# Kernel tuning notes

Hardware: AMD Instinct MI355X
Metric: run time of the kernel (lower is better)

The kernel has to match this reference:

```python
import jax, jax.numpy as jnp
import numpy as np

N, T, F = 4096, 24, 16          # nodes, seq_len, in_features
H = 128                          # temporal_hidden
NH, DO = 4, 32                   # gat num_heads, gat out_features (NH*DO == H)
SEM, PH = 64, 32                 # semantic hidden, predictor hidden
SLOPE = 0.2                      # leaky_relu negative slope
ADJ_P = 0.01                     # adjacency density


def setup_inputs() -> dict:
    key = jax.random.key(0)
    ks = jax.random.split(key, 40)
    f32 = jnp.float32

    def rn(k, shape, s=0.02):
        return jax.random.normal(k, shape, f32) * s

    features = jax.random.normal(ks[0], (N, T, F), f32)
    pos_adj = (jax.random.uniform(ks[1], (N, N)) < ADJ_P).astype(f32)
    neg_adj = (jax.random.uniform(ks[2], (N, N)) < ADJ_P).astype(f32)

    inp = dict(features=features, pos_adj=pos_adj, neg_adj=neg_adj)
    # GRU (torch layout: W_ih [3H,F], W_hh [3H,H], gate order r,z,n)
    inp['gru_Wih'] = rn(ks[3], (3 * H, F), 1.0 / np.sqrt(H))
    inp['gru_Whh'] = rn(ks[4], (3 * H, H), 1.0 / np.sqrt(H))
    inp['gru_bih'] = rn(ks[5], (3 * H,), 1.0 / np.sqrt(H))
    inp['gru_bhh'] = rn(ks[6], (3 * H,), 1.0 / np.sqrt(H))
    # GAT params (linear weights stored [in, out] so we use x @ W)
    i = 7
    for pre in ('pos', 'neg'):
        inp[pre + '_W'] = rn(ks[i], (H, NH * DO)); i += 1
        inp[pre + '_u'] = rn(ks[i], (NH, DO, 1), 1.0); i += 1
        inp[pre + '_v'] = rn(ks[i], (NH, DO, 1), 1.0); i += 1
        inp[pre + '_b'] = rn(ks[i], (1, NH * DO)); i += 1
        inp[pre + '_pW'] = rn(ks[i], (H, NH * DO)); i += 1
        inp[pre + '_pb'] = jnp.zeros((NH * DO,), f32)
    inp['self_W'] = rn(ks[i], (H, H)); i += 1
    inp['self_b'] = jnp.zeros((H,), f32)
    inp['mpos_W'] = rn(ks[i], (NH * DO, H)); i += 1
    inp['mpos_b'] = jnp.zeros((H,), f32)
    inp['mneg_W'] = rn(ks[i], (NH * DO, H)); i += 1
    inp['mneg_b'] = jnp.zeros((H,), f32)
    inp['sem_W1'] = rn(ks[i], (H, SEM)); i += 1
    inp['sem_b1'] = jnp.zeros((SEM,), f32)
    inp['sem_W2'] = rn(ks[i], (SEM, 1)); i += 1
    inp['pred_W1'] = rn(ks[i], (H, PH)); i += 1
    inp['pred_b1'] = jnp.zeros((PH,), f32)
    inp['pred_W2'] = rn(ks[i], (PH, 1)); i += 1
    inp['pred_b2'] = jnp.zeros((1,), f32)
    return inp


def _gru_last(x, Wih, Whh, bih, bhh):
    # x: [N, T, F] -> last hidden state [N, H]
    gi_all = jnp.einsum('ntf,gf->tng', x, Wih) + bih  # precompute input gates [T,N,3H]
    h0 = jnp.zeros((x.shape[0], Whh.shape[1]), x.dtype)

    def step(h, gi):
        gh = h @ Whh.T + bhh
        ir, iz, in_ = jnp.split(gi, 3, axis=-1)
        hr, hz, hn = jnp.split(gh, 3, axis=-1)
        r = jax.nn.sigmoid(ir + hr)
        z = jax.nn.sigmoid(iz + hz)
        n = jnp.tanh(in_ + r * hn)
        return (1.0 - z) * n + z * h, None

    h, _ = jax.lax.scan(step, h0, gi_all)
    return h


def _gat(x, adj, W, u, v, b, pW, pb):
    sup = (x @ W).reshape(-1, NH, DO).transpose(1, 0, 2)     # [NH, N, DO]
    f1 = jnp.matmul(sup, u).reshape(NH, 1, -1)               # [NH, 1, N]
    f2 = jnp.matmul(sup, v).reshape(NH, -1, 1)               # [NH, N, 1]
    w = jax.nn.leaky_relu(f1 + f2, SLOPE)                    # [NH, N, N]
    mw = w * adj                                             # mask
    rs = mw.sum(axis=2, keepdims=True)
    rs = jnp.where(rs == 0, jnp.ones_like(rs), rs)
    attn = mw / rs
    out = jnp.matmul(attn, sup).transpose(1, 0, 2).reshape(-1, NH * DO)
    return out + b + x @ pW + pb                             # bias + residual


def _pairnorm_si(x):
    x = x - x.mean(axis=0)
    rn = jnp.sqrt(1e-6 + (x * x).sum(axis=1, keepdims=True))
    return x / rn


def reference(features, pos_adj, neg_adj,
              gru_Wih, gru_Whh, gru_bih, gru_bhh,
              pos_W, pos_u, pos_v, pos_b, pos_pW, pos_pb,
              neg_W, neg_u, neg_v, neg_b, neg_pW, neg_pb,
              self_W, self_b, mpos_W, mpos_b, mneg_W, mneg_b,
              sem_W1, sem_b1, sem_W2,
              pred_W1, pred_b1, pred_W2, pred_b2):
    support = _gru_last(features, gru_Wih, gru_Whh, gru_bih, gru_bhh)  # [N, H]
    pos_sup = _gat(support, pos_adj, pos_W, pos_u, pos_v, pos_b, pos_pW, pos_pb)
    neg_sup = _gat(support, neg_adj, neg_W, neg_u, neg_v, neg_b, neg_pW, neg_pb)
    self_e = support @ self_W + self_b
    pos_e = pos_sup @ mpos_W + mpos_b
    neg_e = neg_sup @ mneg_W + mneg_b
    emb = jnp.stack([self_e, pos_e, neg_e], axis=1)          # [N, 3, H]
    w = jnp.tanh(emb @ sem_W1 + sem_b1) @ sem_W2             # [N, 3, 1]
    beta = jax.nn.softmax(w, axis=1)
    fused = (beta * emb).sum(axis=1)                          # [N, H]
    fused = _pairnorm_si(fused)
    h = jax.nn.relu(fused @ pred_W1 + pred_b1)               # dropout is eval no-op
    out = jax.nn.sigmoid(h @ pred_W2 + pred_b2).squeeze(-1)  # [N]
    return out
```

## Files before the change

### kernel.cpp

```cpp
#include <hip/hip_runtime.h>


#define NN 4096

typedef unsigned short u16;
typedef unsigned int   u32;
typedef unsigned long long u64;
typedef __attribute__((ext_vector_type(8))) short  short8;
typedef __attribute__((ext_vector_type(4))) float  float4v;

__device__ inline float bf2f(u16 u){ return __uint_as_float(((u32)u)<<16); }
__device__ inline u16 f2bf(float f){
  u32 x = __float_as_uint(f);
  return (u16)((x + 0x7fffu + ((x>>16)&1u))>>16);
}
__device__ inline float ldm(const void* p, int i, int bf){
  return bf ? bf2f(((const u16*)p)[i]) : ((const float*)p)[i];
}
__device__ inline u16 ldm16(const void* p, int i, int bf){
  return bf ? ((const u16*)p)[i] : f2bf(((const float*)p)[i]);
}
__device__ inline float fexp(float x){
  x = fminf(fmaxf(x,-80.f),80.f);
  return __builtin_amdgcn_exp2f(x*1.4426950408889634f);
}
__device__ inline float sigm(float x){
  return __builtin_amdgcn_rcpf(1.f + fexp(-x));
}
__device__ inline float tanhf_(float x){
  float c = fminf(fmaxf(x,-15.f),15.f);
  float e = __builtin_amdgcn_exp2f(c*2.8853900817779268f);
  return (e-1.f)*__builtin_amdgcn_rcpf(e+1.f);
}
__device__ inline float4v mfma16(short8 a, short8 b, float4v c){
  return __builtin_amdgcn_mfma_f32_16x16x32_bf16(a,b,c,0,0,0);
}
__device__ inline int rdbf(const int* __restrict__ mflag){
  int b=0;
  #pragma unroll
  for (int k=0;k<16;k++) b|=mflag[k];
  return b;
}

__global__ __launch_bounds__(256) void k_detect(const u32* __restrict__ adj,
                                                int* __restrict__ mflag)
{
  __shared__ u32 w4[4];
  const int lane=threadIdx.x&63, wv=threadIdx.x>>6;
  int i = (blockIdx.x*256 + threadIdx.x)*4;
  uint4 v = *(const uint4*)(adj + i);
  u32 acc = (v.x | v.y | v.z | v.w) & 0xFFFFu;
  unsigned long long b = __ballot(acc != 0);
  if (lane==0) w4[wv] = (b!=0);
  __syncthreads();
  if (threadIdx.x==0) mflag[blockIdx.x] = (w4[0]|w4[1]|w4[2]|w4[3]) ? 1 : 0;
}

__global__ __launch_bounds__(256) void k_imp(
  const int* __restrict__ mflag,
  const void* gWih, const void* gWhh, const void* gbih, const void* gbhh,
  const void* posW, const void* posu, const void* posv, const void* posb,
  const void* pospW, const void* pospb,
  const void* negW, const void* negu, const void* negv, const void* negb,
  const void* negpW, const void* negpb,
  const void* selfW, const void* selfb, const void* mposW, const void* mposb,
  const void* mnegW, const void* mnegb,
  const void* semW1, const void* semb1, const void* semW2,
  const void* predW1, const void* predb1, const void* predW2, const void* predb2,
  u16* __restrict__ Wihb, u16* __restrict__ Whhb,
  u16* __restrict__ WT1,  u16* __restrict__ WT2,
  float* __restrict__ cbrz, float* __restrict__ cbin, float* __restrict__ cbhn,
  float* __restrict__ cuv,  float* __restrict__ cgb,  float* __restrict__ csb,
  float* __restrict__ cw1,  float* __restrict__ cb1,  float* __restrict__ cw2,
  float* __restrict__ cpw1, float* __restrict__ cpb1, float* __restrict__ cpw2,
  float* __restrict__ cpb2, float* __restrict__ meanacc)
{
  const int bf = rdbf(mflag);
  int i = blockIdx.x*256 + threadIdx.x;
  if (i < 6144){ Wihb[i]=ldm16(gWih,i,bf); return; }  i-=6144;
  if (i < 49152){ Whhb[i]=ldm16(gWhh,i,bf); return; } i-=49152;
  if (i < 81920){
    int m=i>>7,k=i&127,sel=m>>7,ml=m&127;
    const void* s = sel==0?posW: sel==1?pospW: sel==2?negW: sel==3?negpW: selfW;
    WT1[i]=ldm16(s,k*128+ml,bf); return;
  } i-=81920;
  if (i < 32768){
    int m=i>>7,k=i&127;
    const void* s = (m<128)? mposW : mnegW;
    WT2[i]=ldm16(s,k*128+(m&127),bf); return;
  } i-=32768;
  if (i < 256){ cbrz[i]=ldm(gbih,i,bf)+ldm(gbhh,i,bf); return; } i-=256;
  if (i < 128){ cbin[i]=ldm(gbih,256+i,bf); return; } i-=128;
  if (i < 128){ cbhn[i]=ldm(gbhh,256+i,bf); return; } i-=128;
  if (i < 512){
    int s=i>>8, rem=i&255, wh=rem>>7, hd=rem&127;
    const void* p = s? (wh? negv:negu) : (wh? posv:posu);
    cuv[i]=ldm(p,hd,bf); return;
  } i-=512;
  if (i < 256){
    int s=i>>7, d=i&127;
    cgb[i]=ldm(s?negb:posb,d,bf)+ldm(s?negpb:pospb,d,bf); return;
  } i-=256;
  if (i < 384){
    int t=i>>7, d=i&127;
    const void* p = t==0? selfb : t==1? mposb : mnegb;
    csb[i]=ldm(p,d,bf); return;
  } i-=384;
  if (i < 8192){ cw1[i]=ldm(semW1,i,bf); return; } i-=8192;
  if (i < 64){ cb1[i]=ldm(semb1,i,bf); return; } i-=64;
  if (i < 64){ cw2[i]=ldm(semW2,i,bf); return; } i-=64;
  if (i < 4096){ cpw1[i]=ldm(predW1,i,bf); return; } i-=4096;
  if (i < 32){ cpb1[i]=ldm(predb1,i,bf); return; } i-=32;
  if (i < 32){ cpw2[i]=ldm(predW2,i,bf); return; } i-=32;
  if (i < 1){ cpb2[i]=ldm(predb2,i,bf); return; } i-=1;
  if (i < 128){ meanacc[i]=0.f; return; }
}

__global__ __launch_bounds__(512) void k_fat1(
  const int* __restrict__ mflag,
  const void* posadj, const void* negadj,
  int* __restrict__ deg, u16* __restrict__ idx,
  const void* feat,
  const u16* __restrict__ Wihb, const u16* __restrict__ Whhb,
  const float* __restrict__ cbrz, const float* __restrict__ cbin,
  const float* __restrict__ cbhn,
  const u16* __restrict__ WT1, const float* __restrict__ cuv,
  float* __restrict__ C1, float* __restrict__ f12)
{
  __shared__ __attribute__((aligned(16))) u16 sh_x[16*392];
  __shared__ __attribute__((aligned(16))) u16 hbuf[2][16*136];
  const int bf = rdbf(mflag);
  const int tid=threadIdx.x, lane=tid&63, wv=tid>>6;
  const int bx=blockIdx.x;

  if (bx < 1024){
    const int gid = bx*8 + wv;
    const int s = gid>>12, row = gid&4095;
    const void* adj = s? negadj : posadj;
    u64 mask = 0;
    if (bf){
      const u16* rp = (const u16*)adj + (size_t)row*4096;
      #pragma unroll
      for (int it=0; it<8; it++){
        const uint4 vv = *(const uint4*)(rp + it*512 + lane*8);
        u32 w[4]={vv.x,vv.y,vv.z,vv.w};
        #pragma unroll
        for (int q=0;q<4;q++){
          if (w[q]&0xffffu) mask |= 1ull<<(it*8+2*q);
          if (w[q]>>16)     mask |= 1ull<<(it*8+2*q+1);
        }
      }
    } else {
      const float* rp = (const float*)adj + (size_t)row*4096;
      #pragma unroll
      for (int it=0; it<16; it++){
        const uint4 vv = *(const uint4*)(rp + it*256 + lane*4);
        if (vv.x) mask |= 1ull<<(it*4+0);
        if (vv.y) mask |= 1ull<<(it*4+1);
        if (vv.z) mask |= 1ull<<(it*4+2);
        if (vv.w) mask |= 1ull<<(it*4+3);
      }
    }
    int cnt = __popcll(mask);
    int pre = cnt;
    #pragma unroll
    for (int off=1; off<64; off<<=1){
      int o = __shfl_up(pre, off);
      if (lane>=off) pre += o;
    }
    int base_p = pre - cnt;
    int total = __shfl(pre, 63);
    u16* out = idx + ((size_t)s*NN + row)*128;
    u64 mm = mask; int k = 0;
    while (mm){
      int b = __ffsll(mm)-1; mm &= mm-1;
      int e = bf ? ((b>>3)*512 + lane*8 + (b&7))
                 : ((b>>2)*256 + lane*4 + (b&3));
      int p = base_p + k; k++;
      if (p<128) out[p] = (u16)e;
    }
    if (lane==0) deg[s*NN+row] = total>128 ? 128 : total;
    return;
  }

  const int quad=lane>>4, c15=lane&15;
  const int n0=(bx-1024)*16;

  if (bf){
    const u16* f16p=(const u16*)feat;
    for (int i=tid;i<16*384;i+=512){ int n=i/384,e=i-n*384; sh_x[n*392+e]=f16p[(size_t)(n0+n)*384+e]; }
  } else {
    const float* f32p=(const float*)feat;
    for (int i=tid;i<16*384;i+=512){ int n=i/384,e=i-n*384; sh_x[n*392+e]=f2bf(f32p[(size_t)(n0+n)*384+e]); }
  }
  for (int i=tid;i<16*136;i+=512) hbuf[0][i]=0;

  const short8 z8={0,0,0,0,0,0,0,0};
  const float4v z4={0.f,0.f,0.f,0.f};
  short8 bh[3][4], bx3[3];
  #pragma unroll
  for (int g=0;g<3;g++){
    int rowb=(g*8+wv)*16+c15;
    #pragma unroll
    for (int ks=0;ks<4;ks++) bh[g][ks]=*(const short8*)(Whhb+(size_t)rowb*128+ks*32+quad*8);
    bx3[g] = (quad<2)? *(const short8*)(Wihb+(size_t)rowb*16+quad*8) : z8;
  }
  const int j0=wv*16+c15;
  const float brz_r=cbrz[j0], brz_z=cbrz[128+j0];
  const float bin0=cbin[j0],  bhn0=cbhn[j0];
  float hr[4]={0.f,0.f,0.f,0.f};
  __syncthreads();

  for (int t=0;t<24;t++){
    const u16* hb  = hbuf[t&1];
    u16*       hbn = hbuf[(t+1)&1];
    short8 ah[4];
    #pragma unroll
    for (int ks=0;ks<4;ks++) ah[ks]=*(const short8*)(hb + c15*136 + ks*32 + quad*8);
    short8 ax = (quad<2)? *(const short8*)(sh_x + c15*392 + t*16 + quad*8) : z8;
    float4v racc = mfma16(ax,bx3[0],z4);
    float4v zacc = mfma16(ax,bx3[1],z4);
    float4v ni   = mfma16(ax,bx3[2],z4);
    float4v nh   = z4;
    #pragma unroll
    for (int ks=0;ks<4;ks++){
      racc = mfma16(ah[ks],bh[0][ks],racc);
      zacc = mfma16(ah[ks],bh[1][ks],zacc);
      nh   = mfma16(ah[ks],bh[2][ks],nh);
    }
    #pragma unroll
    for (int rr=0;rr<4;rr++){
      const int node = quad*4+rr;
      float r_ = sigm(racc[rr]+brz_r);
      float z_ = sigm(zacc[rr]+brz_z);
      float n_ = tanhf_(ni[rr]+bin0 + r_*(nh[rr]+bhn0));
      float hv = (1.f-z_)*n_ + z_*hr[rr];
      hr[rr]=hv; hbn[node*136+j0]=f2bf(hv);
    }
    __syncthreads();
  }
  short8 a[4];
  #pragma unroll
  for (int ks=0;ks<4;ks++) a[ks]=*(const short8*)(hbuf[0]+c15*136+ks*32+quad*8);
  #pragma unroll
  for (int q=0;q<5;q++){
    int tile=wv*5+q;
    float4v acc={0.f,0.f,0.f,0.f};
    #pragma unroll
    for (int ks=0;ks<4;ks++){
      short8 b=*(const short8*)(WT1+(size_t)(tile*16+c15)*128+ks*32+quad*8);
      acc=mfma16(a[ks],b,acc);
    }
    #pragma unroll
    for (int r=0;r<4;r++) C1[(size_t)(n0+quad*4+r)*640 + tile*16 + c15]=acc[r];
  }
  __syncthreads();
  {
    int q=tid;
    int nl=q&15, h=(q>>4)&3, wsel=(q>>6)&1, s=(q>>7)&1;
    const float* uvp = cuv + s*256 + wsel*128 + h*32;
    const float* SL  = C1 + (size_t)(n0+nl)*640 + s*256 + h*32;
    float t=0.f;
    #pragma unroll
    for (int d=0;d<32;d++) t += SL[d]*uvp[d];
    f12[s*32768 + wsel*16384 + h*4096 + (n0+nl)] = t;
  }
}

__global__ __launch_bounds__(1024) void k_fat2(
  const float* __restrict__ C1, const float* __restrict__ f12,
  const int* __restrict__ deg, const u16* __restrict__ idx,
  const float* __restrict__ cgb, const u16* __restrict__ WT2,
  float* __restrict__ E)
{
  __shared__ u16   nbuf[16][128];
  __shared__ float wbuf[16][4][128];
  __shared__ __attribute__((aligned(16))) u16 sA[16*136];
  const int s=blockIdx.y;
  const int wv=threadIdx.x>>6, lane=threadIdx.x&63;
  const int n0=blockIdx.x*16;
  const int i=n0+wv;
  const int d0=lane, d1=lane+64, h0=lane>>5, h1=2+(lane>>5);
  const float* f1 = f12 + s*32768;
  const float* f2 = f12 + s*32768 + 16384;
  const int dgr = deg[s*NN+i];
  const int dg  = dgr>128 ? 128 : dgr;
  const u16* nb = idx + ((size_t)s*NN+i)*128;
  ((u32*)nbuf[wv])[lane] = ((const u32*)nb)[lane];
  float f2v[4];
  #pragma unroll
  for (int h=0;h<4;h++) f2v[h]=f2[h*4096+i];
  for (int e=lane; e<dg; e+=64){
    int j = nbuf[wv][e];
    #pragma unroll
    for (int h=0;h<4;h++){
      float w = f1[h*4096+j] + f2v[h];
      wbuf[wv][h][e] = w>0.f ? w : 0.2f*w;
    }
  }
  float acc0=0.f,acc1=0.f,rs0=0.f,rs1=0.f;
  #pragma unroll 4
  for (int e=0;e<dg;e++){
    float w0 = wbuf[wv][h0][e];
    float w1 = wbuf[wv][h1][e];
    int j = nbuf[wv][e];
    const float* SL = C1 + (size_t)j*640 + s*256;
    acc0 += w0*SL[d0]; rs0 += w0;
    acc1 += w1*SL[d1]; rs1 += w1;
  }
  if (rs0==0.f) rs0=1.f;
  if (rs1==0.f) rs1=1.f;
  const float* P = C1 + (size_t)i*640 + s*256 + 128;
  sA[wv*136+d0]=f2bf(acc0/rs0 + cgb[s*128+d0] + P[d0]);
  sA[wv*136+d1]=f2bf(acc1/rs1 + cgb[s*128+d1] + P[d1]);
  __syncthreads();
  if (wv<8){
    const int quad=lane>>4, c15=lane&15;
    short8 a[4];
    #pragma unroll
    for (int ks=0;ks<4;ks++) a[ks]=*(const short8*)(sA+c15*136+ks*32+quad*8);
    const int tile=wv;
    float4v acc={0.f,0.f,0.f,0.f};
    #pragma unroll
    for (int ks=0;ks<4;ks++){
      short8 b=*(const short8*)(WT2+(size_t)(s*128+tile*16+c15)*128+ks*32+quad*8);
      acc=mfma16(a[ks],b,acc);
    }
    #pragma unroll
    for (int r=0;r<4;r++) E[(size_t)(n0+quad*4+r)*256 + s*128 + tile*16 + c15]=acc[r];
  }
}

__global__ __launch_bounds__(256) void k_sem(
  const float* __restrict__ C1, const float* __restrict__ E,
  const float* __restrict__ csb, const float* __restrict__ cw1,
  const float* __restrict__ cb1, const float* __restrict__ cw2,
  float* __restrict__ fused, float* __restrict__ meanacc)
{
  __shared__ float sW1[128*64];
  __shared__ float sW2[64];
  __shared__ float sb1[64];
  __shared__ float sE[4][3][128];
  const int tid=threadIdx.x, wv=tid>>6, lane=tid&63;
  for (int i=tid;i<8192;i+=256) sW1[i]=cw1[i];
  if (tid<64){ sW2[tid]=cw2[tid]; sb1[tid]=cb1[tid]; }
  const int n = blockIdx.x*4 + wv;
  for (int d=lane; d<128; d+=64){
    sE[wv][0][d] = C1[(size_t)n*640+512+d] + csb[d];
    sE[wv][1][d] = E[(size_t)n*256 + d]    + csb[128+d];
    sE[wv][2][d] = E[(size_t)n*256+128+d]  + csb[256+d];
  }
  __syncthreads();
  float sc[3];
  #pragma unroll
  for (int s=0;s<3;s++){
    float t = sb1[lane];
    for (int k=0;k<128;k++) t += sE[wv][s][k]*sW1[k*64+lane];
    t = tanhf_(t);
    float p = t*sW2[lane];
    #pragma unroll
    for (int off=32; off; off>>=1) p += __shfl_xor(p, off);
    sc[s]=p;
  }
  float mx = fmaxf(sc[0], fmaxf(sc[1],sc[2]));
  float e0=fexp(sc[0]-mx), e1=fexp(sc[1]-mx), e2=fexp(sc[2]-mx);
  float inv = 1.f/(e0+e1+e2);
  float b0=e0*inv, b1=e1*inv, b2=e2*inv;
  float fv[2];
  for (int h=0; h<2; h++){
    int d=lane+h*64;
    fv[h] = b0*sE[wv][0][d] + b1*sE[wv][1][d] + b2*sE[wv][2][d];
    fused[(size_t)n*128+d] = fv[h];
  }
  __syncthreads();
  for (int h=0; h<2; h++) sE[wv][0][lane+h*64] = fv[h];
  __syncthreads();
  if (tid<128)
    atomicAdd(&meanacc[tid], sE[0][0][tid]+sE[1][0][tid]+sE[2][0][tid]+sE[3][0][tid]);
}

__global__ __launch_bounds__(256) void k_pred(
  const float* __restrict__ fused, const float* __restrict__ meanacc,
  const float* __restrict__ cpw1, const float* __restrict__ cpb1,
  const float* __restrict__ cpw2, const float* __restrict__ cpb2,
  float* __restrict__ out)
{
  __shared__ float sy[4][128];
  __shared__ float sW1[128*32];
  __shared__ float sW2[32];
  const int tid=threadIdx.x, wv=tid>>6, lane=tid&63;
  for (int i=tid;i<4096;i+=256) sW1[i]=cpw1[i];
  if (tid<32) sW2[tid]=cpw2[tid];
  const int n = blockIdx.x*4 + wv;
  const float inv_n = 1.f/4096.f;
  float x0 = fused[(size_t)n*128+lane]    - meanacc[lane]*inv_n;
  float x1 = fused[(size_t)n*128+64+lane] - meanacc[64+lane]*inv_n;
  float ss = x0*x0 + x1*x1;
  #pragma unroll
  for (int o=32;o;o>>=1) ss += __shfl_xor(ss,o);
  float ir = 1.f/sqrtf(1e-6f + ss);
  sy[wv][lane]=x0*ir; sy[wv][64+lane]=x1*ir;
  __syncthreads();
  float h=0.f;
  if (lane<32){
    h = cpb1[lane];
    for (int k=0;k<128;k++) h += sy[wv][k]*sW1[k*32+lane];
    h = h>0.f? h : 0.f;
    h = h*sW2[lane];
  }
  #pragma unroll
  for (int o=32;o;o>>=1) h += __shfl_xor(h,o);
  if (!lane){
    float z = h + cpb2[0];
    out[n] = __builtin_amdgcn_rcpf(1.f + fexp(-z));
  }
}

extern "C" void kernel_launch(void* const* d_in, const int* in_sizes, int n_in,
                              void* d_out, int out_size, void* d_ws, size_t ws_size,
                              hipStream_t stream)
{
  const void* feat  =d_in[0];
  const void* posadj=d_in[1];
  const void* negadj=d_in[2];
  const void* gWih  =d_in[3];
  const void* gWhh  =d_in[4];
  const void* gbih  =d_in[5];
  const void* gbhh  =d_in[6];
  const void* posW  =d_in[7];
  const void* posu  =d_in[8];
  const void* posv  =d_in[9];
  const void* posb  =d_in[10];
  const void* pospW =d_in[11];
  const void* pospb =d_in[12];
  const void* negW  =d_in[13];
  const void* negu  =d_in[14];
  const void* negv  =d_in[15];
  const void* negb  =d_in[16];
  const void* negpW =d_in[17];
  const void* negpb =d_in[18];
  const void* selfW =d_in[19];
  const void* selfb =d_in[20];
  const void* mposW =d_in[21];
  const void* mposb =d_in[22];
  const void* mnegW =d_in[23];
  const void* mnegb =d_in[24];
  const void* semW1 =d_in[25];
  const void* semb1 =d_in[26];
  const void* semW2 =d_in[27];
  const void* predW1=d_in[28];
  const void* predb1=d_in[29];
  const void* predW2=d_in[30];
  const void* predb2=d_in[31];

  char* wsb=(char*)d_ws; size_t off=0;
  auto alloc=[&](size_t bytes)->void*{ void* p=wsb+off; off+=(bytes+255)&~(size_t)255; return p; };
  int*   mflag=(int*)  alloc(256);
  u16*   Wihb =(u16*)  alloc(6144*2);
  u16*   Whhb =(u16*)  alloc(49152*2);
  u16*   WT1  =(u16*)  alloc(81920*2);
  u16*   WT2  =(u16*)  alloc(32768*2);
  float* cbrz =(float*)alloc(256*4);
  float* cbin =(float*)alloc(128*4);
  float* cbhn =(float*)alloc(128*4);
  float* cuv  =(float*)alloc(512*4);
  float* cgb  =(float*)alloc(256*4);
  float* csb  =(float*)alloc(384*4);
  float* cw1  =(float*)alloc(8192*4);
  float* cb1  =(float*)alloc(64*4);
  float* cw2  =(float*)alloc(64*4);
  float* cpw1 =(float*)alloc(4096*4);
  float* cpb1 =(float*)alloc(32*4);
  float* cpw2 =(float*)alloc(32*4);
  float* cpb2 =(float*)alloc(4);
  float* C1   =(float*)alloc((size_t)NN*640*4);
  float* f12  =(float*)alloc((size_t)65536*4);
  int*   deg  =(int*)  alloc((size_t)2*NN*4);
  u16*   nidx =(u16*)  alloc((size_t)2*NN*128*2);
  float* E    =(float*)alloc((size_t)NN*256*4);
  float* fused=(float*)alloc((size_t)NN*128*4);
  float* meanacc=(float*)alloc(128*4);
  (void)ws_size; (void)in_sizes; (void)n_in; (void)out_size;

  k_detect<<<16,          256,0,stream>>>((const u32*)posadj,mflag);
  k_imp   <<<720,         256,0,stream>>>(mflag,gWih,gWhh,gbih,gbhh,
              posW,posu,posv,posb,pospW,pospb,negW,negu,negv,negb,negpW,negpb,
              selfW,selfb,mposW,mposb,mnegW,mnegb,semW1,semb1,semW2,
              predW1,predb1,predW2,predb2,
              Wihb,Whhb,WT1,WT2,cbrz,cbin,cbhn,cuv,cgb,csb,cw1,cb1,cw2,
              cpw1,cpb1,cpw2,cpb2,meanacc);
  k_fat1  <<<1280,        512,0,stream>>>(mflag,posadj,negadj,deg,nidx,
              feat,Wihb,Whhb,cbrz,cbin,cbhn,WT1,cuv,C1,f12);
  k_fat2  <<<dim3(256,2),1024,0,stream>>>(C1,f12,deg,nidx,cgb,WT2,E);
  k_sem   <<<NN/4,        256,0,stream>>>(C1,E,csb,cw1,cb1,cw2,fused,meanacc);
  k_pred  <<<NN/4,        256,0,stream>>>(fused,meanacc,cpw1,cpb1,cpw2,cpb2,(float*)d_out);
}
```

Measured before the change: 318.8 us.

## Split CSR build from GRU kernel, store C1 in bf16, vectorize sem/pred matvecs

Adjacency-to-neighbour-list extraction moves into its own kernel. Each wave scans half a row and reserves output slots with an atomicAdd on deg, which k_detect now zeroes. The GRU/projection kernel writes the C1 intermediate as bf16 instead of fp32, halving its store and gather traffic in the GAT and semantic kernels. The semantic and predictor weights are pre-transposed with padding so the matvecs use float4 LDS reads, and k_sem handles four nodes per wave with a block-level mean reduction. The costs are extra bf16 rounding, nondeterministic neighbour order, no clamp on deg at 128, and losing the overlap between CSR building and GRU work that the fused launch gave.

```diff
diff --git a/kernel.cpp b/kernel.cpp
--- a/kernel.cpp
+++ b/kernel.cpp
@@ -43,7 +43,8 @@
 }
 
 __global__ __launch_bounds__(256) void k_detect(const u32* __restrict__ adj,
-                                                int* __restrict__ mflag)
+                                                int* __restrict__ mflag,
+                                                int* __restrict__ deg)
 {
   __shared__ u32 w4[4];
   const int lane=threadIdx.x&63, wv=threadIdx.x>>6;
@@ -52,6 +53,8 @@
   u32 acc = (v.x | v.y | v.z | v.w) & 0xFFFFu;
   unsigned long long b = __ballot(acc != 0);
   if (lane==0) w4[wv] = (b!=0);
+  deg[blockIdx.x*512 + threadIdx.x] = 0;
+  deg[blockIdx.x*512 + threadIdx.x + 256] = 0;
   __syncthreads();
   if (threadIdx.x==0) mflag[blockIdx.x] = (w4[0]|w4[1]|w4[2]|w4[3]) ? 1 : 0;
 }
@@ -71,8 +74,8 @@
   u16* __restrict__ WT1,  u16* __restrict__ WT2,
   float* __restrict__ cbrz, float* __restrict__ cbin, float* __restrict__ cbhn,
   float* __restrict__ cuv,  float* __restrict__ cgb,  float* __restrict__ csb,
-  float* __restrict__ cw1,  float* __restrict__ cb1,  float* __restrict__ cw2,
-  float* __restrict__ cpw1, float* __restrict__ cpb1, float* __restrict__ cpw2,
+  float* __restrict__ cw1t, float* __restrict__ cb1,  float* __restrict__ cw2,
+  float* __restrict__ cpw1t, float* __restrict__ cpb1, float* __restrict__ cpw2,
   float* __restrict__ cpb2, float* __restrict__ meanacc)
 {
   const int bf = rdbf(mflag);
@@ -106,85 +109,92 @@
     const void* p = t==0? selfb : t==1? mposb : mnegb;
     csb[i]=ldm(p,d,bf); return;
   } i-=384;
-  if (i < 8192){ cw1[i]=ldm(semW1,i,bf); return; } i-=8192;
+  if (i < 8448){
+    int c=i/132, k=i-c*132;
+    cw1t[i] = (k<128)? ldm(semW1,k*64+c,bf) : 0.f; return;
+  } i-=8448;
   if (i < 64){ cb1[i]=ldm(semb1,i,bf); return; } i-=64;
   if (i < 64){ cw2[i]=ldm(semW2,i,bf); return; } i-=64;
-  if (i < 4096){ cpw1[i]=ldm(predW1,i,bf); return; } i-=4096;
+  if (i < 4224){
+    int c=i/132, k=i-c*132;
+    cpw1t[i] = (k<128)? ldm(predW1,k*32+c,bf) : 0.f; return;
+  } i-=4224;
   if (i < 32){ cpb1[i]=ldm(predb1,i,bf); return; } i-=32;
   if (i < 32){ cpw2[i]=ldm(predW2,i,bf); return; } i-=32;
   if (i < 1){ cpb2[i]=ldm(predb2,i,bf); return; } i-=1;
   if (i < 128){ meanacc[i]=0.f; return; }
 }
 
-__global__ __launch_bounds__(512) void k_fat1(
+__global__ __launch_bounds__(256) void k_csr(
   const int* __restrict__ mflag,
   const void* posadj, const void* negadj,
-  int* __restrict__ deg, u16* __restrict__ idx,
-  const void* feat,
+  int* __restrict__ deg, u16* __restrict__ idx)
+{
+  const int bf = rdbf(mflag);
+  const int s = blockIdx.y;
+  const void* adj = s? negadj : posadj;
+  const int lane = threadIdx.x&63;
+  const int hr   = blockIdx.x*4 + (threadIdx.x>>6);
+  const int row  = hr>>1, half = hr&1;
+  u32 mask = 0;
+  if (bf){
+    const u16* rp = (const u16*)adj + (size_t)row*4096 + half*2048;
+    #pragma unroll
+    for (int q=0;q<4;q++){
+      uint4 v = *(const uint4*)(rp + q*512 + lane*8);
+      if (v.x&0xffffu) mask|=1u<<(q*8+0); if (v.x>>16) mask|=1u<<(q*8+1);
+      if (v.y&0xffffu) mask|=1u<<(q*8+2); if (v.y>>16) mask|=1u<<(q*8+3);
+      if (v.z&0xffffu) mask|=1u<<(q*8+4); if (v.z>>16) mask|=1u<<(q*8+5);
+      if (v.w&0xffffu) mask|=1u<<(q*8+6); if (v.w>>16) mask|=1u<<(q*8+7);
+    }
+  } else {
+    const float* rp = (const float*)adj + (size_t)row*4096 + half*2048;
+    #pragma unroll
+    for (int q=0;q<8;q++){
+      uint4 v = *(const uint4*)(rp + q*256 + lane*4);
+      if (v.x) mask|=1u<<(q*4+0);
+      if (v.y) mask|=1u<<(q*4+1);
+      if (v.z) mask|=1u<<(q*4+2);
+      if (v.w) mask|=1u<<(q*4+3);
+    }
+  }
+  int cnt = __popc(mask);
+  int pre = cnt;
+  #pragma unroll
+  for (int off=1; off<64; off<<=1){
+    int o = __shfl_up(pre, off);
+    if (lane>=off) pre += o;
+  }
+  int tot = __shfl(pre, 63);
+  int wbase = 0;
+  if (lane==0) wbase = atomicAdd(&deg[s*NN+row], tot);
+  wbase = __shfl(wbase, 0);
+  int base_p = wbase + pre - cnt;
+  u16* out = idx + ((size_t)s*NN + row)*128;
+  u32 mm = mask; int k = 0;
+  while (mm){
+    int b = __ffs(mm)-1; mm &= mm-1;
+    int e = bf ? (half*2048 + (b>>3)*512 + lane*8 + (b&7))
+               : (half*2048 + (b>>2)*256 + lane*4 + (b&3));
+    int p = base_p + k; k++;
+    if (p<128) out[p] = (u16)e;
+  }
+}
+
+__global__ __launch_bounds__(512) void k_gruf(
+  const int* __restrict__ mflag, const void* feat,
   const u16* __restrict__ Wihb, const u16* __restrict__ Whhb,
   const float* __restrict__ cbrz, const float* __restrict__ cbin,
   const float* __restrict__ cbhn,
   const u16* __restrict__ WT1, const float* __restrict__ cuv,
-  float* __restrict__ C1, float* __restrict__ f12)
+  u16* __restrict__ C1b, float* __restrict__ f12)
 {
   __shared__ __attribute__((aligned(16))) u16 sh_x[16*392];
   __shared__ __attribute__((aligned(16))) u16 hbuf[2][16*136];
   const int bf = rdbf(mflag);
   const int tid=threadIdx.x, lane=tid&63, wv=tid>>6;
-  const int bx=blockIdx.x;
-
-  if (bx < 1024){
-    const int gid = bx*8 + wv;
-    const int s = gid>>12, row = gid&4095;
-    const void* adj = s? negadj : posadj;
-    u64 mask = 0;
-    if (bf){
-      const u16* rp = (const u16*)adj + (size_t)row*4096;
-      #pragma unroll
-      for (int it=0; it<8; it++){
-        const uint4 vv = *(const uint4*)(rp + it*512 + lane*8);
-        u32 w[4]={vv.x,vv.y,vv.z,vv.w};
-        #pragma unroll
-        for (int q=0;q<4;q++){
-          if (w[q]&0xffffu) mask |= 1ull<<(it*8+2*q);
-          if (w[q]>>16)     mask |= 1ull<<(it*8+2*q+1);
-        }
-      }
-    } else {
-      const float* rp = (const float*)adj + (size_t)row*4096;
-      #pragma unroll
-      for (int it=0; it<16; it++){
-        const uint4 vv = *(const uint4*)(rp + it*256 + lane*4);
-        if (vv.x) mask |= 1ull<<(it*4+0);
-        if (vv.y) mask |= 1ull<<(it*4+1);
-        if (vv.z) mask |= 1ull<<(it*4+2);
-        if (vv.w) mask |= 1ull<<(it*4+3);
-      }
-    }
-    int cnt = __popcll(mask);
-    int pre = cnt;
-    #pragma unroll
-    for (int off=1; off<64; off<<=1){
-      int o = __shfl_up(pre, off);
-      if (lane>=off) pre += o;
-    }
-    int base_p = pre - cnt;
-    int total = __shfl(pre, 63);
-    u16* out = idx + ((size_t)s*NN + row)*128;
-    u64 mm = mask; int k = 0;
-    while (mm){
-      int b = __ffsll(mm)-1; mm &= mm-1;
-      int e = bf ? ((b>>3)*512 + lane*8 + (b&7))
-                 : ((b>>2)*256 + lane*4 + (b&3));
-      int p = base_p + k; k++;
-      if (p<128) out[p] = (u16)e;
-    }
-    if (lane==0) deg[s*NN+row] = total>128 ? 128 : total;
-    return;
-  }
-
   const int quad=lane>>4, c15=lane&15;
-  const int n0=(bx-1024)*16;
+  const int n0=blockIdx.x*16;
 
   if (bf){
     const u16* f16p=(const u16*)feat;
@@ -252,23 +262,24 @@
       acc=mfma16(a[ks],b,acc);
     }
     #pragma unroll
-    for (int r=0;r<4;r++) C1[(size_t)(n0+quad*4+r)*640 + tile*16 + c15]=acc[r];
+    for (int r=0;r<4;r++)
+      C1b[(size_t)(n0+quad*4+r)*640 + tile*16 + c15]=f2bf(acc[r]);
   }
   __syncthreads();
   {
     int q=tid;
     int nl=q&15, h=(q>>4)&3, wsel=(q>>6)&1, s=(q>>7)&1;
     const float* uvp = cuv + s*256 + wsel*128 + h*32;
-    const float* SL  = C1 + (size_t)(n0+nl)*640 + s*256 + h*32;
+    const u16*   SL  = C1b + (size_t)(n0+nl)*640 + s*256 + h*32;
     float t=0.f;
     #pragma unroll
-    for (int d=0;d<32;d++) t += SL[d]*uvp[d];
+    for (int d=0;d<32;d++) t += bf2f(SL[d])*uvp[d];
     f12[s*32768 + wsel*16384 + h*4096 + (n0+nl)] = t;
   }
 }
 
-__global__ __launch_bounds__(1024) void k_fat2(
-  const float* __restrict__ C1, const float* __restrict__ f12,
+__global__ __launch_bounds__(1024) void k_gat2(
+  const u16* __restrict__ C1b, const float* __restrict__ f12,
   const int* __restrict__ deg, const u16* __restrict__ idx,
   const float* __restrict__ cgb, const u16* __restrict__ WT2,
   float* __restrict__ E)
@@ -304,15 +315,15 @@
     float w0 = wbuf[wv][h0][e];
     float w1 = wbuf[wv][h1][e];
     int j = nbuf[wv][e];
-    const float* SL = C1 + (size_t)j*640 + s*256;
-    acc0 += w0*SL[d0]; rs0 += w0;
-    acc1 += w1*SL[d1]; rs1 += w1;
+    const u16* SL = C1b + (size_t)j*640 + s*256;
+    acc0 += w0*bf2f(SL[d0]); rs0 += w0;
+    acc1 += w1*bf2f(SL[d1]); rs1 += w1;
   }
   if (rs0==0.f) rs0=1.f;
   if (rs1==0.f) rs1=1.f;
-  const float* P = C1 + (size_t)i*640 + s*256 + 128;
-  sA[wv*136+d0]=f2bf(acc0/rs0 + cgb[s*128+d0] + P[d0]);
-  sA[wv*136+d1]=f2bf(acc1/rs1 + cgb[s*128+d1] + P[d1]);
+  const u16* P = C1b + (size_t)i*640 + s*256 + 128;
+  sA[wv*136+d0]=f2bf(acc0/rs0 + cgb[s*128+d0] + bf2f(P[d0]));
+  sA[wv*136+d1]=f2bf(acc1/rs1 + cgb[s*128+d1] + bf2f(P[d1]));
   __syncthreads();
   if (wv<8){
     const int quad=lane>>4, c15=lane&15;
@@ -332,64 +343,72 @@
 }
 
 __global__ __launch_bounds__(256) void k_sem(
-  const float* __restrict__ C1, const float* __restrict__ E,
-  const float* __restrict__ csb, const float* __restrict__ cw1,
+  const u16* __restrict__ C1b, const float* __restrict__ E,
+  const float* __restrict__ csb, const float* __restrict__ cw1t,
   const float* __restrict__ cb1, const float* __restrict__ cw2,
   float* __restrict__ fused, float* __restrict__ meanacc)
 {
-  __shared__ float sW1[128*64];
+  __shared__ float sW1t[64*132];
   __shared__ float sW2[64];
   __shared__ float sb1[64];
   __shared__ float sE[4][3][128];
+  __shared__ float redm[4][128];
   const int tid=threadIdx.x, wv=tid>>6, lane=tid&63;
-  for (int i=tid;i<8192;i+=256) sW1[i]=cw1[i];
+  for (int i=tid;i<8448;i+=256) sW1t[i]=cw1t[i];
   if (tid<64){ sW2[tid]=cw2[tid]; sb1[tid]=cb1[tid]; }
-  const int n = blockIdx.x*4 + wv;
-  for (int d=lane; d<128; d+=64){
-    sE[wv][0][d] = C1[(size_t)n*640+512+d] + csb[d];
-    sE[wv][1][d] = E[(size_t)n*256 + d]    + csb[128+d];
-    sE[wv][2][d] = E[(size_t)n*256+128+d]  + csb[256+d];
-  }
-  __syncthreads();
-  float sc[3];
-  #pragma unroll
-  for (int s=0;s<3;s++){
-    float t = sb1[lane];
-    for (int k=0;k<128;k++) t += sE[wv][s][k]*sW1[k*64+lane];
-    t = tanhf_(t);
-    float p = t*sW2[lane];
-    #pragma unroll
-    for (int off=32; off; off>>=1) p += __shfl_xor(p, off);
-    sc[s]=p;
-  }
-  float mx = fmaxf(sc[0], fmaxf(sc[1],sc[2]));
-  float e0=fexp(sc[0]-mx), e1=fexp(sc[1]-mx), e2=fexp(sc[2]-mx);
-  float inv = 1.f/(e0+e1+e2);
-  float b0=e0*inv, b1=e1*inv, b2=e2*inv;
-  float fv[2];
-  for (int h=0; h<2; h++){
-    int d=lane+h*64;
-    fv[h] = b0*sE[wv][0][d] + b1*sE[wv][1][d] + b2*sE[wv][2][d];
-    fused[(size_t)n*128+d] = fv[h];
-  }
-  __syncthreads();
-  for (int h=0; h<2; h++) sE[wv][0][lane+h*64] = fv[h];
+  __syncthreads();
+  const float* wcol = sW1t + lane*132;
+  float macc0=0.f, macc1=0.f;
+  for (int u=0;u<4;u++){
+    const int n = blockIdx.x*16 + wv*4 + u;
+    for (int d=lane; d<128; d+=64){
+      sE[wv][0][d] = bf2f(C1b[(size_t)n*640+512+d]) + csb[d];
+      sE[wv][1][d] = E[(size_t)n*256 + d]    + csb[128+d];
+      sE[wv][2][d] = E[(size_t)n*256+128+d]  + csb[256+d];
+    }
+    float sc[3];
+    #pragma unroll
+    for (int s=0;s<3;s++){
+      float t = sb1[lane];
+      #pragma unroll
+      for (int k=0;k<128;k+=4){
+        float4 e4 = *(const float4*)&sE[wv][s][k];
+        float4 w4 = *(const float4*)&wcol[k];
+        t += e4.x*w4.x + e4.y*w4.y + e4.z*w4.z + e4.w*w4.w;
+      }
+      t = tanhf_(t);
+      float p = t*sW2[lane];
+      #pragma unroll
+      for (int off=32; off; off>>=1) p += __shfl_xor(p, off);
+      sc[s]=p;
+    }
+    float mx = fmaxf(sc[0], fmaxf(sc[1],sc[2]));
+    float e0=fexp(sc[0]-mx), e1=fexp(sc[1]-mx), e2=fexp(sc[2]-mx);
+    float inv = 1.f/(e0+e1+e2);
+    float b0=e0*inv, b1=e1*inv, b2=e2*inv;
+    float f0 = b0*sE[wv][0][lane]    + b1*sE[wv][1][lane]    + b2*sE[wv][2][lane];
+    float f1 = b0*sE[wv][0][lane+64] + b1*sE[wv][1][lane+64] + b2*sE[wv][2][lane+64];
+    fused[(size_t)n*128+lane]    = f0;
+    fused[(size_t)n*128+64+lane] = f1;
+    macc0 += f0; macc1 += f1;
+  }
+  redm[wv][lane]=macc0; redm[wv][lane+64]=macc1;
   __syncthreads();
   if (tid<128)
-    atomicAdd(&meanacc[tid], sE[0][0][tid]+sE[1][0][tid]+sE[2][0][tid]+sE[3][0][tid]);
+    atomicAdd(&meanacc[tid], redm[0][tid]+redm[1][tid]+redm[2][tid]+redm[3][tid]);
 }
 
 __global__ __launch_bounds__(256) void k_pred(
   const float* __restrict__ fused, const float* __restrict__ meanacc,
-  const float* __restrict__ cpw1, const float* __restrict__ cpb1,
+  const float* __restrict__ cpw1t, const float* __restrict__ cpb1,
   const float* __restrict__ cpw2, const float* __restrict__ cpb2,
   float* __restrict__ out)
 {
   __shared__ float sy[4][128];
-  __shared__ float sW1[128*32];
+  __shared__ float sW1t[32*132];
   __shared__ float sW2[32];
   const int tid=threadIdx.x, wv=tid>>6, lane=tid&63;
-  for (int i=tid;i<4096;i+=256) sW1[i]=cpw1[i];
+  for (int i=tid;i<4224;i+=256) sW1t[i]=cpw1t[i];
   if (tid<32) sW2[tid]=cpw2[tid];
   const int n = blockIdx.x*4 + wv;
   const float inv_n = 1.f/4096.f;
@@ -401,17 +420,24 @@
   float ir = 1.f/sqrtf(1e-6f + ss);
   sy[wv][lane]=x0*ir; sy[wv][64+lane]=x1*ir;
   __syncthreads();
+  const int c = lane&31, half = lane>>5;
+  const float* wcol = sW1t + c*132 + half*64;
+  const float* yrow = sy[wv] + half*64;
   float h=0.f;
-  if (lane<32){
-    h = cpb1[lane];
-    for (int k=0;k<128;k++) h += sy[wv][k]*sW1[k*32+lane];
-    h = h>0.f? h : 0.f;
-    h = h*sW2[lane];
-  }
-  #pragma unroll
-  for (int o=32;o;o>>=1) h += __shfl_xor(h,o);
+  #pragma unroll
+  for (int k=0;k<64;k+=4){
+    float4 y4 = *(const float4*)&yrow[k];
+    float4 w4 = *(const float4*)&wcol[k];
+    h += y4.x*w4.x + y4.y*w4.y + y4.z*w4.z + y4.w*w4.w;
+  }
+  h += __shfl_xor(h,32);
+  h += cpb1[c];
+  h = h>0.f? h : 0.f;
+  float p = h*sW2[c];
+  #pragma unroll
+  for (int o=16;o;o>>=1) p += __shfl_xor(p,o);
   if (!lane){
-    float z = h + cpb2[0];
+    float z = p + cpb2[0];
     out[n] = __builtin_amdgcn_rcpf(1.f + fexp(-z));
   }
 }
@@ -466,14 +492,14 @@
   float* cuv  =(float*)alloc(512*4);
   float* cgb  =(float*)alloc(256*4);
   float* csb  =(float*)alloc(384*4);
-  float* cw1  =(float*)alloc(8192*4);
+  float* cw1t =(float*)alloc(8448*4);
   float* cb1  =(float*)alloc(64*4);
   float* cw2  =(float*)alloc(64*4);
-  float* cpw1 =(float*)alloc(4096*4);
+  float* cpw1t=(float*)alloc(4224*4);
   float* cpb1 =(float*)alloc(32*4);
   float* cpw2 =(float*)alloc(32*4);
   float* cpb2 =(float*)alloc(4);
-  float* C1   =(float*)alloc((size_t)NN*640*4);
+  u16*   C1b  =(u16*)  alloc((size_t)NN*640*2);
   float* f12  =(float*)alloc((size_t)65536*4);
   int*   deg  =(int*)  alloc((size_t)2*NN*4);
   u16*   nidx =(u16*)  alloc((size_t)2*NN*128*2);
@@ -482,16 +508,17 @@
   float* meanacc=(float*)alloc(128*4);
   (void)ws_size; (void)in_sizes; (void)n_in; (void)out_size;
 
-  k_detect<<<16,          256,0,stream>>>((const u32*)posadj,mflag);
-  k_imp   <<<720,         256,0,stream>>>(mflag,gWih,gWhh,gbih,gbhh,
+  k_detect<<<16,          256,0,stream>>>((const u32*)posadj,mflag,deg);
+  k_imp   <<<722,         256,0,stream>>>(mflag,gWih,gWhh,gbih,gbhh,
               posW,posu,posv,posb,pospW,pospb,negW,negu,negv,negb,negpW,negpb,
               selfW,selfb,mposW,mposb,mnegW,mnegb,semW1,semb1,semW2,
               predW1,predb1,predW2,predb2,
-              Wihb,Whhb,WT1,WT2,cbrz,cbin,cbhn,cuv,cgb,csb,cw1,cb1,cw2,
-              cpw1,cpb1,cpw2,cpb2,meanacc);
-  k_fat1  <<<1280,        512,0,stream>>>(mflag,posadj,negadj,deg,nidx,
-              feat,Wihb,Whhb,cbrz,cbin,cbhn,WT1,cuv,C1,f12);
-  k_fat2  <<<dim3(256,2),1024,0,stream>>>(C1,f12,deg,nidx,cgb,WT2,E);
-  k_sem   <<<NN/4,        256,0,stream>>>(C1,E,csb,cw1,cb1,cw2,fused,meanacc);
-  k_pred  <<<NN/4,        256,0,stream>>>(fused,meanacc,cpw1,cpb1,cpw2,cpb2,(float*)d_out);
-}
+              Wihb,Whhb,WT1,WT2,cbrz,cbin,cbhn,cuv,cgb,csb,cw1t,cb1,cw2,
+              cpw1t,cpb1,cpw2,cpb2,meanacc);
+  k_csr   <<<dim3(2048,2),256,0,stream>>>(mflag,posadj,negadj,deg,nidx);
+  k_gruf  <<<NN/16,       512,0,stream>>>(mflag,feat,Wihb,Whhb,cbrz,cbin,cbhn,
+                                          WT1,cuv,C1b,f12);
+  k_gat2  <<<dim3(256,2),1024,0,stream>>>(C1b,f12,deg,nidx,cgb,WT2,E);
+  k_sem   <<<NN/16,       256,0,stream>>>(C1b,E,csb,cw1t,cb1,cw2,fused,meanacc);
+  k_pred  <<<NN/4,        256,0,stream>>>(fused,meanacc,cpw1t,cpb1,cpw2,cpb2,(float*)d_out);
+}
```

Result: faster. 293.9 us (-7.8%).
